# Optimization experiments

Measured on AMD Instinct MI355X. Metric: run time of the kernel, lower is better.

The kernel has to match this reference:

```python
import jax, jax.numpy as jnp
import numpy as np

B, L_SRC, H = 16, 2048, 1024


def setup_inputs() -> dict:
    key = jax.random.key(0)
    ks = jax.random.split(key, 12)
    s = 1.0 / np.sqrt(H)
    return {
        "query": jax.random.normal(ks[0], (B, 1, H), jnp.float32),
        "states": jax.random.normal(ks[1], (B, L_SRC, H), jnp.float32),
        "states_features": jax.random.normal(ks[2], (B, L_SRC, H), jnp.float32),
        "coverage": jax.random.uniform(ks[3], (B, L_SRC, 1), jnp.float32),
        "source_mask": jax.random.randint(ks[4], (B, L_SRC), 0, 2, jnp.int32),
        "is_coverage": 1,
        "Wq": jax.random.normal(ks[5], (H, H), jnp.float32) * s,
        "bq": jax.random.normal(ks[6], (H,), jnp.float32) * s,
        "Wc": jax.random.normal(ks[7], (1, H), jnp.float32) * s,
        "v": jax.random.normal(ks[8], (H, 1), jnp.float32) * s,
        "Wout": jax.random.normal(ks[9], (H, 2 * H), jnp.float32) * s,
        "bout": jax.random.normal(ks[10], (H,), jnp.float32) * s,
    }


def reference(query, states, states_features, coverage, source_mask, is_coverage,
              Wq, bq, Wc, v, Wout, bout):
    # query: (B,1,H); states/states_features: (B,L,H); coverage: (B,L,1)
    query_features = query @ Wq.T + bq                       # (B,1,H), broadcasts over L
    total = query_features + states_features                 # (B,L,H)
    if is_coverage:
        total = total + coverage @ Wc                        # Linear(1,H), no bias
    alignments = jnp.tanh(total) @ v                         # (B,L,1)
    mask = source_mask.astype(bool)[:, :, None]              # (B,L,1)
    alignments = jnp.where(mask, alignments, -jnp.inf)
    align_vectors = jax.nn.softmax(alignments, axis=1)       # softmax over L_src
    c = jnp.einsum('bls,blh->bsh', align_vectors, states)    # (B,1,H)
    concat_c = jnp.concatenate([c, query], axis=2)           # (B,1,2H)
    attn_h = concat_c @ Wout.T + bout                         # (B,1,H)
    new_coverage = coverage + align_vectors
    return attn_h, new_coverage, align_vectors
```

## Files before the change

### kernel.cpp

```cpp
#include <hip/hip_runtime.h>
#include <cfloat>

#define HD 1024
#define LS 2048
#define NB 16
#define LCHUNK 64
#define LPER   (LS / LCHUNK)

struct f4 { float x, y, z, w; };

__device__ inline f4 ld4(const float* p) { return *reinterpret_cast<const f4*>(p); }

__device__ inline float ftanh(float x) {
    x = fminf(10.f, fmaxf(-10.f, x));
    float t = __expf(2.f * x);
    return 1.f - 2.f * __builtin_amdgcn_rcpf(t + 1.f);
}

__device__ inline float dotTanh(const f4& s, const f4& q, const f4& wc, const f4& v, float covs) {
    return ftanh(s.x + q.x + covs * wc.x) * v.x
         + ftanh(s.y + q.y + covs * wc.y) * v.y
         + ftanh(s.z + q.z + covs * wc.z) * v.z
         + ftanh(s.w + q.w + covs * wc.w) * v.w;
}

__device__ inline float waveReduce(float v) {
    #pragma unroll
    for (int off = 32; off; off >>= 1) v += __shfl_xor(v, off, 64);
    return v;
}

__global__ void qf_kernel(const float* __restrict__ query, const float* __restrict__ Wq,
                          const float* __restrict__ bq, float* __restrict__ qf) {
    int h = blockIdx.x;
    int tid = threadIdx.x;
    int wv = tid >> 6, lane = tid & 63;
    int k0 = tid * 4;
    f4 w = ld4(Wq + (size_t)h * HD + k0);
    __shared__ float red[4][NB];
    float acc[NB];
    #pragma unroll
    for (int b = 0; b < NB; ++b) {
        f4 q = ld4(query + b * HD + k0);
        acc[b] = w.x * q.x + w.y * q.y + w.z * q.z + w.w * q.w;
    }
    #pragma unroll
    for (int b = 0; b < NB; ++b) {
        float r = waveReduce(acc[b]);
        if (lane == 0) red[wv][b] = r;
    }
    __syncthreads();
    if (tid < NB) {
        float s = red[0][tid] + red[1][tid] + red[2][tid] + red[3][tid];
        qf[tid * HD + h] = s + bq[h];
    }
}

__global__ __launch_bounds__(256) void energy_kernel(
    const float* __restrict__ sf, const float* __restrict__ qf,
    const float* __restrict__ Wc, const float* __restrict__ vv,
    const float* __restrict__ coverage, const int* __restrict__ mask,
    const int* __restrict__ is_cov_p, float* __restrict__ e_out)
{
    int b = blockIdx.x >> 7;
    int wv = threadIdx.x >> 6, lane = threadIdx.x & 63;
    int rbase = (blockIdx.x & 127) * 16 + wv * 4;
    int l4 = lane * 4;
    int covflag = *is_cov_p;
    int row0 = b * LS + rbase;

    int4 mk = *reinterpret_cast<const int4*>(mask + row0);
    bool mA = mk.x != 0, mB = mk.y != 0, mC = mk.z != 0, mD = mk.w != 0;

    float covA = 0.f, covB = 0.f, covC = 0.f, covD = 0.f;
    if (covflag) {
        if (mA) covA = coverage[row0 + 0];
        if (mB) covB = coverage[row0 + 1];
        if (mC) covC = coverage[row0 + 2];
        if (mD) covD = coverage[row0 + 3];
    }

    const float* qfr = qf + b * HD + l4;
    const float* pA = sf + (size_t)row0 * HD + l4;
    float accA = 0.f, accB = 0.f, accC = 0.f, accD = 0.f;

    #pragma unroll
    for (int it = 0; it < 4; ++it) {
        int o = it * 256;
        f4 q  = ld4(qfr + o);
        f4 wc = ld4(Wc + o + l4);
        f4 vf = ld4(vv + o + l4);
        f4 sA, sB, sC, sD;
        if (mA) sA = ld4(pA + o);
        if (mB) sB = ld4(pA + HD + o);
        if (mC) sC = ld4(pA + 2 * HD + o);
        if (mD) sD = ld4(pA + 3 * HD + o);
        if (mA) accA += dotTanh(sA, q, wc, vf, covA);
        if (mB) accB += dotTanh(sB, q, wc, vf, covB);
        if (mC) accC += dotTanh(sC, q, wc, vf, covC);
        if (mD) accD += dotTanh(sD, q, wc, vf, covD);
    }

    #pragma unroll
    for (int off = 32; off; off >>= 1) {
        accA += __shfl_xor(accA, off, 64);
        accB += __shfl_xor(accB, off, 64);
        accC += __shfl_xor(accC, off, 64);
        accD += __shfl_xor(accD, off, 64);
    }
    if (lane == 0) {
        f4 o;
        o.x = mA ? accA : -1e30f;
        o.y = mB ? accB : -1e30f;
        o.z = mC ? accC : -1e30f;
        o.w = mD ? accD : -1e30f;
        *reinterpret_cast<f4*>(e_out + row0) = o;
    }
}

__global__ __launch_bounds__(256) void ctx_kernel(const float* __restrict__ e,
                                                  const float* __restrict__ states,
                                                  float* __restrict__ cpart) {
    int chunk = blockIdx.x;
    int b = blockIdx.y;
    int tid = threadIdx.x;
    __shared__ float wq[LPER];
    __shared__ int ridx[LPER];
    __shared__ int snnz;
    int base_row = b * LS + chunk * LPER;
    if (tid < 64) {
        float ev = (tid < LPER) ? e[base_row + tid] : -1e30f;
        float w = __expf(ev);
        unsigned long long m = __ballot(w != 0.f);
        if (w != 0.f) {
            int pos = __popcll(m & ((1ull << tid) - 1));
            wq[pos] = w;
            ridx[pos] = tid;
        }
        if (tid == 0) snnz = __popcll(m);
    }
    __syncthreads();
    int nnz = snnz;
    int h0 = tid * 4;
    const float* sbase = states + (size_t)base_row * HD + h0;
    float ax = 0.f, ay = 0.f, az = 0.f, aw = 0.f;
    for (int i = 0; i < nnz; i += 4) {
        int j1 = i + 1, j2 = i + 2, j3 = i + 3;
        float w0 = wq[i];
        int   r0 = ridx[i];
        float w1 = (j1 < nnz) ? wq[j1] : 0.f;
        int   r1 = (j1 < nnz) ? ridx[j1] : r0;
        float w2 = (j2 < nnz) ? wq[j2] : 0.f;
        int   r2 = (j2 < nnz) ? ridx[j2] : r0;
        float w3 = (j3 < nnz) ? wq[j3] : 0.f;
        int   r3 = (j3 < nnz) ? ridx[j3] : r0;
        f4 s0 = ld4(sbase + ((size_t)r0 << 10));
        f4 s1 = ld4(sbase + ((size_t)r1 << 10));
        f4 s2 = ld4(sbase + ((size_t)r2 << 10));
        f4 s3 = ld4(sbase + ((size_t)r3 << 10));
        ax = fmaf(w0, s0.x, ax); ay = fmaf(w0, s0.y, ay); az = fmaf(w0, s0.z, az); aw = fmaf(w0, s0.w, aw);
        ax = fmaf(w1, s1.x, ax); ay = fmaf(w1, s1.y, ay); az = fmaf(w1, s1.z, az); aw = fmaf(w1, s1.w, aw);
        ax = fmaf(w2, s2.x, ax); ay = fmaf(w2, s2.y, ay); az = fmaf(w2, s2.z, az); aw = fmaf(w2, s2.w, aw);
        ax = fmaf(w3, s3.x, ax); ay = fmaf(w3, s3.y, ay); az = fmaf(w3, s3.z, az); aw = fmaf(w3, s3.w, aw);
    }
    f4 o; o.x = ax; o.y = ay; o.z = az; o.w = aw;
    *reinterpret_cast<f4*>(cpart + ((size_t)(b * LCHUNK + chunk)) * HD + h0) = o;
}

__global__ __launch_bounds__(1024) void mid_kernel(
    const float* __restrict__ e, const float* __restrict__ coverage,
    const float* __restrict__ cpart, float* __restrict__ scale,
    float* __restrict__ csum, float* __restrict__ out_align, float* __restrict__ out_newcov)
{
    __shared__ float redm[16], reds[16];
    __shared__ float red4[4][256];
    if (blockIdx.x < 16) {
        int b = blockIdx.x;
        int t = threadIdx.x;
        int wv = t >> 6, lane = t & 63;
        float v0 = e[b * LS + t];
        float v1 = e[b * LS + t + 1024];
        float mx = fmaxf(v0, v1);
        #pragma unroll
        for (int off = 32; off; off >>= 1) mx = fmaxf(mx, __shfl_xor(mx, off, 64));
        if (lane == 0) redm[wv] = mx;
        __syncthreads();
        mx = redm[0];
        #pragma unroll
        for (int i = 1; i < 16; ++i) mx = fmaxf(mx, redm[i]);
        float e0 = __expf(v0 - mx), e1 = __expf(v1 - mx);
        float s = e0 + e1;
        #pragma unroll
        for (int off = 32; off; off >>= 1) s += __shfl_xor(s, off, 64);
        if (lane == 0) reds[wv] = s;
        __syncthreads();
        s = 0.f;
        #pragma unroll
        for (int i = 0; i < 16; ++i) s += reds[i];
        float invZ = 1.f / s;
        if (t == 0) scale[b] = __expf(-mx) * invZ;
        int i0 = b * LS + t, i1 = i0 + 1024;
        float p0 = e0 * invZ, p1 = e1 * invZ;
        out_align[i0] = p0;
        out_align[i1] = p1;
        out_newcov[i0] = coverage[i0] + p0;
        out_newcov[i1] = coverage[i1] + p1;
    } else {
        int blk = blockIdx.x - 16;
        int tt = threadIdx.x & 255;
        int g = threadIdx.x >> 8;
        int elem = blk * 256 + tt;
        int b = elem >> 10, h = elem & 1023;
        const float* p = cpart + (((size_t)(b * LCHUNK + g * 16)) << 10) + h;
        float s = 0.f;
        #pragma unroll
        for (int ch = 0; ch < 16; ++ch) s += p[(size_t)ch << 10];
        red4[g][tt] = s;
        __syncthreads();
        if (g == 0) csum[elem] = red4[0][tt] + red4[1][tt] + red4[2][tt] + red4[3][tt];
    }
}

__global__ void out_kernel(const float* __restrict__ csum, const float* __restrict__ query,
                           const float* __restrict__ Wout, const float* __restrict__ bout,
                           const float* __restrict__ scale, float* __restrict__ attn) {
    int h = blockIdx.x;
    int tid = threadIdx.x;
    int wv = tid >> 6, lane = tid & 63;
    int j0 = tid * 8;
    const float* wr = Wout + (size_t)h * (2 * HD);
    f4 w0 = ld4(wr + j0);
    f4 w1 = ld4(wr + j0 + 4);
    const float* src = (j0 < HD) ? (csum + j0) : (query + j0 - HD);
    __shared__ float red[4][NB];
    float acc[NB];
    #pragma unroll
    for (int b = 0; b < NB; ++b) {
        f4 x0 = ld4(src + b * HD);
        f4 x1 = ld4(src + b * HD + 4);
        acc[b] = w0.x * x0.x + w0.y * x0.y + w0.z * x0.z + w0.w * x0.w
               + w1.x * x1.x + w1.y * x1.y + w1.z * x1.z + w1.w * x1.w;
    }
    #pragma unroll
    for (int b = 0; b < NB; ++b) {
        float r = waveReduce(acc[b]);
        if (lane == 0) red[wv][b] = r;
    }
    __syncthreads();
    if (tid < NB) {
        float cpartial = red[0][tid] + red[1][tid];
        float qpartial = red[2][tid] + red[3][tid];
        attn[tid * HD + h] = cpartial * scale[tid] + qpartial + bout[h];
    }
}

extern "C" void kernel_launch(void* const* d_in, const int* in_sizes, int n_in,
                              void* d_out, int out_size, void* d_ws, size_t ws_size,
                              hipStream_t stream) {
    const float* query    = (const float*)d_in[0];
    const float* states   = (const float*)d_in[1];
    const float* sf       = (const float*)d_in[2];
    const float* coverage = (const float*)d_in[3];
    const int*   mask     = (const int*)d_in[4];
    const int*   is_cov   = (const int*)d_in[5];
    const float* Wq       = (const float*)d_in[6];
    const float* bq       = (const float*)d_in[7];
    const float* Wc       = (const float*)d_in[8];
    const float* v        = (const float*)d_in[9];
    const float* Wout     = (const float*)d_in[10];
    const float* bout     = (const float*)d_in[11];

    float* out      = (float*)d_out;
    float* attn     = out;
    float* newcov   = out + 16384;
    float* alignout = out + 49152;

    float* w  = (float*)d_ws;
    float* qf      = w;
    float* e       = w + 16384;
    float* cpart   = w + 49152;
    float* scale   = w + 49152 + 1048576;
    float* csum    = scale + 16;

    qf_kernel<<<dim3(HD), dim3(256), 0, stream>>>(query, Wq, bq, qf);
    energy_kernel<<<dim3(2048), dim3(256), 0, stream>>>(sf, qf, Wc, v, coverage, mask, is_cov, e);
    ctx_kernel<<<dim3(LCHUNK, NB), dim3(256), 0, stream>>>(e, states, cpart);
    mid_kernel<<<dim3(80), dim3(1024), 0, stream>>>(e, coverage, cpart, scale, csum, alignout, newcov);
    out_kernel<<<dim3(HD), dim3(256), 0, stream>>>(csum, query, Wout, bout, scale, attn);
}
```

Before: 59.88 us.

## Fuse energy and context kernels into one per-chunk kernel

Merges the energy computation and the masked context accumulation into a single kernel launched per (chunk, batch). Each block computes energies for its 32 rows (8 rows per wave) and keeps them in shared memory, then directly builds the sparse weight list and accumulates states. This drops one launch and the global round-trip of energies between kernels. The cost is fewer, heavier blocks (1024 instead of 2048 for the energy phase) and more registers per thread, which may lower occupancy and latency hiding.

```diff
diff --git a/kernel.cpp b/kernel.cpp
--- a/kernel.cpp
+++ b/kernel.cpp
@@ -56,33 +56,35 @@
     }
 }
 
-__global__ __launch_bounds__(256) void energy_kernel(
+__global__ __launch_bounds__(256) void fusedEC_kernel(
     const float* __restrict__ sf, const float* __restrict__ qf,
     const float* __restrict__ Wc, const float* __restrict__ vv,
     const float* __restrict__ coverage, const int* __restrict__ mask,
-    const int* __restrict__ is_cov_p, float* __restrict__ e_out)
+    const int* __restrict__ is_cov_p, const float* __restrict__ states,
+    float* __restrict__ e_out, float* __restrict__ cpart)
 {
-    int b = blockIdx.x >> 7;
-    int wv = threadIdx.x >> 6, lane = threadIdx.x & 63;
-    int rbase = (blockIdx.x & 127) * 16 + wv * 4;
+    int chunk = blockIdx.x;
+    int b = blockIdx.y;
+    int tid = threadIdx.x;
+    int wv = tid >> 6, lane = tid & 63;
     int l4 = lane * 4;
+    int base_row = b * LS + chunk * LPER;
+    int row0 = base_row + wv * 8;
+
+    __shared__ float e_loc[LPER];
+
     int covflag = *is_cov_p;
-    int row0 = b * LS + rbase;
-
-    int4 mk = *reinterpret_cast<const int4*>(mask + row0);
-    bool mA = mk.x != 0, mB = mk.y != 0, mC = mk.z != 0, mD = mk.w != 0;
-
-    float covA = 0.f, covB = 0.f, covC = 0.f, covD = 0.f;
-    if (covflag) {
-        if (mA) covA = coverage[row0 + 0];
-        if (mB) covB = coverage[row0 + 1];
-        if (mC) covC = coverage[row0 + 2];
-        if (mD) covD = coverage[row0 + 3];
-    }
+    int4 mk0 = *reinterpret_cast<const int4*>(mask + row0);
+    int4 mk1 = *reinterpret_cast<const int4*>(mask + row0 + 4);
+    bool m[8] = { mk0.x != 0, mk0.y != 0, mk0.z != 0, mk0.w != 0,
+                  mk1.x != 0, mk1.y != 0, mk1.z != 0, mk1.w != 0 };
+    float cov[8];
+    #pragma unroll
+    for (int r = 0; r < 8; ++r) cov[r] = (covflag && m[r]) ? coverage[row0 + r] : 0.f;
 
     const float* qfr = qf + b * HD + l4;
-    const float* pA = sf + (size_t)row0 * HD + l4;
-    float accA = 0.f, accB = 0.f, accC = 0.f, accD = 0.f;
+    const float* ps = sf + (size_t)row0 * HD + l4;
+    float acc[8] = {0.f, 0.f, 0.f, 0.f, 0.f, 0.f, 0.f, 0.f};
 
     #pragma unroll
     for (int it = 0; it < 4; ++it) {
@@ -90,54 +92,45 @@
         f4 q  = ld4(qfr + o);
         f4 wc = ld4(Wc + o + l4);
         f4 vf = ld4(vv + o + l4);
-        f4 sA, sB, sC, sD;
-        if (mA) sA = ld4(pA + o);
-        if (mB) sB = ld4(pA + HD + o);
-        if (mC) sC = ld4(pA + 2 * HD + o);
-        if (mD) sD = ld4(pA + 3 * HD + o);
-        if (mA) accA += dotTanh(sA, q, wc, vf, covA);
-        if (mB) accB += dotTanh(sB, q, wc, vf, covB);
-        if (mC) accC += dotTanh(sC, q, wc, vf, covC);
-        if (mD) accD += dotTanh(sD, q, wc, vf, covD);
+        f4 s[8];
+        #pragma unroll
+        for (int r = 0; r < 8; ++r) if (m[r]) s[r] = ld4(ps + (size_t)r * HD + o);
+        #pragma unroll
+        for (int r = 0; r < 8; ++r) if (m[r]) acc[r] += dotTanh(s[r], q, wc, vf, cov[r]);
     }
 
     #pragma unroll
     for (int off = 32; off; off >>= 1) {
-        accA += __shfl_xor(accA, off, 64);
-        accB += __shfl_xor(accB, off, 64);
-        accC += __shfl_xor(accC, off, 64);
-        accD += __shfl_xor(accD, off, 64);
+        #pragma unroll
+        for (int r = 0; r < 8; ++r) acc[r] += __shfl_xor(acc[r], off, 64);
     }
     if (lane == 0) {
-        f4 o;
-        o.x = mA ? accA : -1e30f;
-        o.y = mB ? accB : -1e30f;
-        o.z = mC ? accC : -1e30f;
-        o.w = mD ? accD : -1e30f;
-        *reinterpret_cast<f4*>(e_out + row0) = o;
-    }
-}
-
-__global__ __launch_bounds__(256) void ctx_kernel(const float* __restrict__ e,
-                                                  const float* __restrict__ states,
-                                                  float* __restrict__ cpart) {
-    int chunk = blockIdx.x;
-    int b = blockIdx.y;
-    int tid = threadIdx.x;
+        float ev[8];
+        #pragma unroll
+        for (int r = 0; r < 8; ++r) ev[r] = m[r] ? acc[r] : -1e30f;
+        f4 o0, o1;
+        o0.x = ev[0]; o0.y = ev[1]; o0.z = ev[2]; o0.w = ev[3];
+        o1.x = ev[4]; o1.y = ev[5]; o1.z = ev[6]; o1.w = ev[7];
+        *reinterpret_cast<f4*>(e_out + row0) = o0;
+        *reinterpret_cast<f4*>(e_out + row0 + 4) = o1;
+        #pragma unroll
+        for (int r = 0; r < 8; ++r) e_loc[wv * 8 + r] = ev[r];
+    }
+    __syncthreads();
+
     __shared__ float wq[LPER];
     __shared__ int ridx[LPER];
     __shared__ int snnz;
-    int base_row = b * LS + chunk * LPER;
     if (tid < 64) {
-        float ev = (tid < LPER) ? e[base_row + tid] : -1e30f;
+        float ev = (tid < LPER) ? e_loc[tid] : -1e30f;
         float w = __expf(ev);
-        unsigned long long m = __ballot(w != 0.f);
+        unsigned long long bm = __ballot(w != 0.f);
         if (w != 0.f) {
-            int pos = __popcll(m & ((1ull << tid) - 1));
+            int pos = __popcll(bm & ((1ull << tid) - 1));
             wq[pos] = w;
             ridx[pos] = tid;
         }
-        if (tid == 0) snnz = __popcll(m);
+        if (tid == 0) snnz = __popcll(bm);
     }
     __syncthreads();
     int nnz = snnz;
@@ -283,8 +276,8 @@
     float* csum    = scale + 16;
 
     qf_kernel<<<dim3(HD), dim3(256), 0, stream>>>(query, Wq, bq, qf);
-    energy_kernel<<<dim3(2048), dim3(256), 0, stream>>>(sf, qf, Wc, v, coverage, mask, is_cov, e);
-    ctx_kernel<<<dim3(LCHUNK, NB), dim3(256), 0, stream>>>(e, states, cpart);
+    fusedEC_kernel<<<dim3(LCHUNK, NB), dim3(256), 0, stream>>>(
+        sf, qf, Wc, v, coverage, mask, is_cov, states, e, cpart);
     mid_kernel<<<dim3(80), dim3(1024), 0, stream>>>(e, coverage, cpart, scale, csum, alignout, newcov);
     out_kernel<<<dim3(HD), dim3(256), 0, stream>>>(csum, query, Wout, bout, scale, attn);
 }
```

Measured after the change: 54.87 us. 1.09x faster.
